# Optimization experiments

Measured on AMD Instinct MI355X. Metric: run time of the kernel, lower is better.

Reference implementation:

```python
import math
import jax, jax.numpy as jnp
import numpy as np

B, T, C, H = 2, 1024, 1024, 16
D = C // H
NEG = -jnp.inf


def setup_inputs() -> dict:
    key = jax.random.key(0)
    ks = jax.random.split(key, 4)
    x_star = jax.random.normal(ks[0], (B, T, C), jnp.float32)
    x_hat = jax.random.normal(ks[1], (B, T, C), jnp.float32)
    # attn_masks semantics: True = keep. star-keys: causal; hat-keys: diagonal only.
    keep_star = jnp.broadcast_to(jnp.tril(jnp.ones((T, T), bool)), (B, T, T))
    keep_hat = jnp.broadcast_to(jnp.eye(T, dtype=bool), (B, T, T))
    W_attn = jax.random.normal(ks[2], (C, 3 * C), jnp.float32) * (1.0 / math.sqrt(C))
    b_attn = jnp.zeros((3 * C,), jnp.float32)
    W_proj = jax.random.normal(ks[3], (C, C), jnp.float32) * (1.0 / math.sqrt(C))
    b_proj = jnp.zeros((C,), jnp.float32)
    return dict(x_star=x_star, x_hat=x_hat, keep_star=keep_star, keep_hat=keep_hat,
                W_attn=W_attn, b_attn=b_attn, W_proj=W_proj, b_proj=b_proj)


def _interleave(x_star, x_hat, keep_star, keep_hat, W_attn, b_attn, W_proj, b_proj):
    def qkv(x):
        q, k, v = jnp.split(x @ W_attn + b_attn, 3, axis=-1)
        r = lambda t: t.reshape(B, T, H, D).transpose(0, 2, 1, 3)  # (B,H,T,D)
        return r(q), r(k), r(v)

    q_s, k_s, v_s = qkv(x_star)
    q_h, k_h, v_h = qkv(x_hat)

    scale = 1.0 / math.sqrt(D)
    attend = lambda q, k: jnp.einsum('bhqd,bhkd->bhqk', q, k) * scale

    # blocking masks (True = block), broadcast over heads
    mask_star = ~keep_star[:, None, :, :]
    mask_hat = ~keep_hat[:, None, :, :]
    mask_causal = ~jnp.tril(jnp.ones((T, T), bool))[None, None]

    def mlp(y):  # (B,H,T,D) -> (B,T,C)
        y = y.transpose(0, 2, 1, 3).reshape(B, T, C)
        return y @ W_proj + b_proj  # resid_dropout is identity in eval

    # star stream: plain causal self-attention
    att_star = jnp.where(mask_causal, NEG, attend(q_s, k_s))
    y_star = mlp(jax.nn.softmax(att_star, axis=-1) @ v_s)

    # hat stream: merge two score streams (hat queries vs star keys / hat keys)
    att_hs = jnp.where(mask_star, NEG, attend(q_h, k_s))
    att_hh = jnp.where(mask_hat, NEG, attend(q_h, k_h))
    merged = jnp.where(jnp.isinf(att_hh), att_hs, att_hh)
    p = jax.nn.softmax(merged, axis=-1)
    y_hat = (jnp.where(mask_star, 0.0, p) @ v_s
             + jnp.where(mask_hat, 0.0, p) @ v_h)
    y_hat = mlp(y_hat)
    return y_star, y_hat


def reference(x_star, x_hat, keep_star, keep_hat, W_attn, b_attn, W_proj, b_proj):
    return _interleave(x_star, x_hat, keep_star, keep_hat, W_attn, b_attn, W_proj, b_proj)
```

## Files before the change

kernel.cpp:

```cpp
#include <hip/hip_runtime.h>
#include <math.h>

#define T_ 1024
#define C_ 1024
#define H_ 16
#define D_ 64
#define B_ 2
#define M2 (B_*T_*C_)
#define QSC 0.18033688f

typedef __attribute__((ext_vector_type(8))) short bf16x8;
typedef __attribute__((ext_vector_type(8))) unsigned short ushort8;
typedef __attribute__((ext_vector_type(4))) float f32x4;

__device__ inline float fast_exp2(float x) {
  return __builtin_amdgcn_exp2f(x);
}

__device__ inline unsigned short f2bf(float f) {
  unsigned int u = __float_as_uint(f);
  u += 0x7fff + ((u >> 16) & 1);
  return (unsigned short)(u >> 16);
}
__device__ inline float bf2f(unsigned short u) {
  return __uint_as_float(((unsigned int)u) << 16);
}
__device__ inline unsigned int pack2bf(float lo, float hi) {
  unsigned int ul = __float_as_uint(lo);
  unsigned int uh = __float_as_uint(hi);
  ul += 0x7fff + ((ul >> 16) & 1);
  uh += 0x7fff + ((uh >> 16) & 1);
  return (ul >> 16) | (uh & 0xffff0000u);
}

__device__ inline void load16(unsigned short* lds, const unsigned short* g) {
  __builtin_amdgcn_global_load_lds(
      (const __attribute__((address_space(1))) unsigned int*)g,
      (__attribute__((address_space(3))) unsigned int*)lds, 16, 0, 0);
}

__device__ void transpose_tile(const float* __restrict__ Win,
                               unsigned short* __restrict__ Wout, int N,
                               int n0, int k0, float (*Ts)[65], int tid)
{
#pragma unroll
  for (int p = 0; p < 4; ++p) {
    int chunk = tid + p * 256;
    int r = chunk >> 4, c4 = chunk & 15;
    float4 v = *(const float4*)(Win + (size_t)(k0 + r) * N + n0 + c4 * 4);
    Ts[r][c4*4+0] = v.x; Ts[r][c4*4+1] = v.y;
    Ts[r][c4*4+2] = v.z; Ts[r][c4*4+3] = v.w;
  }
  __syncthreads();
#pragma unroll
  for (int p = 0; p < 2; ++p) {
    int chunk = tid + p * 256;
    int n = chunk >> 3, kq = chunk & 7;
    ushort8 o;
#pragma unroll
    for (int j = 0; j < 8; ++j) o[j] = f2bf(Ts[kq * 8 + j][n]);
    *(ushort8*)(Wout + (size_t)(n0 + n) * 1024 + k0 + kq * 8) = o;
  }
}

__global__ __launch_bounds__(256) void prepass(
    const float* __restrict__ xs, const float* __restrict__ xh,
    const float* __restrict__ Wa, const float* __restrict__ Wp,
    unsigned short* __restrict__ Xbf, unsigned short* __restrict__ WaT,
    unsigned short* __restrict__ WpT)
{
  __shared__ float Ts[64][65];
  const int bid = blockIdx.x;
  const int tid = threadIdx.x;
  if (bid < 4096) {
    size_t c = (size_t)bid * 256 + tid;
    size_t e = c * 4;
    const float* src = (e < (size_t)2048 * 1024) ? (xs + e)
                                                 : (xh + e - (size_t)2048 * 1024);
    float4 v = *(const float4*)src;
    ushort4 o;
    o.x = f2bf(v.x); o.y = f2bf(v.y); o.z = f2bf(v.z); o.w = f2bf(v.w);
    *(ushort4*)(Xbf + e) = o;
  } else if (bid < 4864) {
    int t = bid - 4096;
    transpose_tile(Wa, WaT, 3072, (t % 48) * 64, (t / 48) * 64, Ts, tid);
  } else {
    int t = bid - 4864;
    transpose_tile(Wp, WpT, 1024, (t % 16) * 64, (t / 16) * 64, Ts, tid);
  }
}

__global__ __launch_bounds__(512) void qkv_mfma(
    const unsigned short* __restrict__ A,
    const unsigned short* __restrict__ Bt,
    const float* __restrict__ bias,
    unsigned short* __restrict__ qkv)
{
  __shared__ __align__(16) unsigned short As[128 * 64];
  __shared__ __align__(16) unsigned short Bs[128 * 64];
  const int tid = threadIdx.x;
  const int col0 = blockIdx.x * 128;
  const int row0 = blockIdx.y * 128;
  const int w = tid >> 6, lane = tid & 63;
  const int lane16 = lane & 15, quad = lane >> 4;
  const int wm = w >> 2, wn = w & 3;
  f32x4 acc[4][2];
#pragma unroll
  for (int mt = 0; mt < 4; ++mt)
#pragma unroll
    for (int nt = 0; nt < 2; ++nt) acc[mt][nt] = (f32x4){0.f, 0.f, 0.f, 0.f};

  for (int k0 = 0; k0 < 1024; k0 += 64) {
    __syncthreads();
#pragma unroll
    for (int it = 0; it < 2; ++it) {
      int chunk = tid + it * 512;
      int row = chunk >> 3, cq = chunk & 7, gq = cq ^ (row & 7);
      load16(As + chunk * 8, A  + (size_t)(row0 + row) * 1024 + k0 + gq * 8);
      load16(Bs + chunk * 8, Bt + (size_t)(col0 + row) * 1024 + k0 + gq * 8);
    }
    __syncthreads();
#pragma unroll
    for (int kb = 0; kb < 2; ++kb) {
      bf16x8 af[4], bfr[2];
      int q = kb * 4 + quad;
#pragma unroll
      for (int mt = 0; mt < 4; ++mt) {
        int m = wm * 64 + mt * 16 + lane16;
        af[mt] = *(const bf16x8*)&As[m * 64 + (q ^ (m & 7)) * 8];
      }
#pragma unroll
      for (int nt = 0; nt < 2; ++nt) {
        int n = wn * 32 + nt * 16 + lane16;
        bfr[nt] = *(const bf16x8*)&Bs[n * 64 + (q ^ (n & 7)) * 8];
      }
#pragma unroll
      for (int mt = 0; mt < 4; ++mt)
#pragma unroll
        for (int nt = 0; nt < 2; ++nt)
          acc[mt][nt] = __builtin_amdgcn_mfma_f32_16x16x32_bf16(
              af[mt], bfr[nt], acc[mt][nt], 0, 0, 0);
    }
  }

#pragma unroll
  for (int mt = 0; mt < 4; ++mt) {
#pragma unroll
    for (int nt = 0; nt < 2; ++nt) {
      int gn = col0 + wn * 32 + nt * 16 + lane16;
      int which = gn >> 10, c = gn & 1023;
      int h = c >> 6, d = c & 63;
      float bv = bias[gn];
#pragma unroll
      for (int r = 0; r < 4; ++r) {
        int gm = row0 + wm * 64 + mt * 16 + quad * 4 + r;
        int s = gm >> 11, b = (gm >> 10) & 1, t = gm & 1023;
        float val = acc[mt][nt][r] + bv;
        if (which == 0) val *= QSC;
        size_t idx;
        if (which == 2 && s == 0)
          idx = (size_t)2 * M2 + ((size_t)(b * 16 + h) * 64 + d) * 1024 + t;
        else
          idx = (size_t)(s * 3 + which) * M2 +
                ((size_t)(b * 16 + h) * 1024 + t) * 64 + d;
        qkv[idx] = f2bf(val);
      }
    }
  }
}

__global__ __launch_bounds__(256) void proj_mfma(
    const unsigned short* __restrict__ A,
    const unsigned short* __restrict__ Bt,
    const float* __restrict__ bias,
    float* __restrict__ out)
{
  __shared__ __align__(16) unsigned short As[128 * 64];
  __shared__ __align__(16) unsigned short Bs[64 * 64];
  const int tid = threadIdx.x;
  const int col0 = blockIdx.x * 64;
  const int row0 = blockIdx.y * 128;
  const int w = tid >> 6, lane = tid & 63;
  const int lane16 = lane & 15, quad = lane >> 4;
  const int wm = w >> 1, wn = w & 1;
  f32x4 acc[4][2];
#pragma unroll
  for (int mt = 0; mt < 4; ++mt)
#pragma unroll
    for (int nt = 0; nt < 2; ++nt) acc[mt][nt] = (f32x4){0.f, 0.f, 0.f, 0.f};

  for (int k0 = 0; k0 < 1024; k0 += 64) {
    __syncthreads();
#pragma unroll
    for (int it = 0; it < 4; ++it) {
      int chunk = tid + it * 256;
      int row = chunk >> 3, cq = chunk & 7, gq = cq ^ (row & 7);
      load16(As + chunk * 8, A + (size_t)(row0 + row) * 1024 + k0 + gq * 8);
    }
#pragma unroll
    for (int it = 0; it < 2; ++it) {
      int chunk = tid + it * 256;
      int row = chunk >> 3, cq = chunk & 7, gq = cq ^ (row & 7);
      load16(Bs + chunk * 8, Bt + (size_t)(col0 + row) * 1024 + k0 + gq * 8);
    }
    __syncthreads();
#pragma unroll
    for (int kb = 0; kb < 2; ++kb) {
      bf16x8 af[4], bfr[2];
      int q = kb * 4 + quad;
#pragma unroll
      for (int mt = 0; mt < 4; ++mt) {
        int m = wm * 64 + mt * 16 + lane16;
        af[mt] = *(const bf16x8*)&As[m * 64 + (q ^ (m & 7)) * 8];
      }
#pragma unroll
      for (int nt = 0; nt < 2; ++nt) {
        int n = wn * 32 + nt * 16 + lane16;
        bfr[nt] = *(const bf16x8*)&Bs[n * 64 + (q ^ (n & 7)) * 8];
      }
#pragma unroll
      for (int mt = 0; mt < 4; ++mt)
#pragma unroll
        for (int nt = 0; nt < 2; ++nt)
          acc[mt][nt] = __builtin_amdgcn_mfma_f32_16x16x32_bf16(
              af[mt], bfr[nt], acc[mt][nt], 0, 0, 0);
    }
  }

#pragma unroll
  for (int mt = 0; mt < 4; ++mt) {
#pragma unroll
    for (int nt = 0; nt < 2; ++nt) {
      int gn = col0 + wn * 32 + nt * 16 + lane16;
      float bv = bias[gn];
#pragma unroll
      for (int r = 0; r < 4; ++r) {
        int gm = row0 + wm * 64 + mt * 16 + quad * 4 + r;
        out[(size_t)gm * 1024 + gn] = acc[mt][nt][r] + bv;
      }
    }
  }
}

__global__ __launch_bounds__(256) void attn_kernel(
    const unsigned short* __restrict__ ws, unsigned short* __restrict__ Y)
{
  __shared__ __align__(16) unsigned short Qs[64 * 64];
  __shared__ __align__(16) unsigned short Ks[2][64 * 64];
  __shared__ __align__(16) unsigned short Vts[2][64 * 64];
  __shared__ __align__(16) unsigned short Ps[4][16][72];
  __shared__ float diag[64];

  const int tid = threadIdx.x;
  const int bx  = blockIdx.x;
  const int inner = bx & 63;
  const int h = inner & 15;
  const int b = (inner >> 4) & 1;
  const int s = (inner >> 5) & 1;
  const int qt = 15 - (bx >> 6);
  const int i0 = qt * 64;
  const size_t hb = (size_t)(b * H_ + h) * T_ * D_;

  const unsigned short* Qg  = ws + (size_t)(s ? 3 : 0) * M2 + hb;
  const unsigned short* Kg  = ws + (size_t)1 * M2 + hb;
  const unsigned short* VTg = ws + (size_t)2 * M2 + hb;
  const unsigned short* Khg = ws + (size_t)4 * M2 + hb;
  const unsigned short* Vhg = ws + (size_t)5 * M2 + hb;

  const int lane = tid & 63;
  const int w = tid >> 6;
  const int lane16 = lane & 15, quad = lane >> 4;
  const int wq0 = w * 16;

#pragma unroll
  for (int it = 0; it < 2; ++it) {
    int ch = tid + it * 256;
    int row = ch >> 3, cq = ch & 7, gq = cq ^ (row & 7);
    load16(Qs + ch * 8, Qg + (size_t)(i0 + row) * 64 + gq * 8);
    load16(&Ks[0][ch * 8], Kg + (size_t)(0 * 64 + row) * 64 + gq * 8);
    load16(&Vts[0][ch * 8], VTg + (size_t)row * 1024 + 0 * 64 + gq * 8);
  }
  __syncthreads();

  bf16x8 qf[2];
  {
    int m = wq0 + lane16;
    qf[0] = *(const bf16x8*)&Qs[m * 64 + ((quad) ^ (m & 7)) * 8];
    qf[1] = *(const bf16x8*)&Qs[m * 64 + ((4 + quad) ^ (m & 7)) * 8];
  }
  if (s == 1) {
    if (tid < 64) {
      const unsigned short* kh = Khg + (size_t)(i0 + tid) * 64;
      float sum = 0.f;
#pragma unroll
      for (int c = 0; c < 8; ++c) {
        bf16x8 qv = *(const bf16x8*)&Qs[tid * 64 + (c ^ (tid & 7)) * 8];
        ushort8 kv = *(const ushort8*)(kh + c * 8);
#pragma unroll
        for (int j = 0; j < 8; ++j)
          sum += bf2f((unsigned short)qv[j]) * bf2f(kv[j]);
      }
      diag[tid] = sum;
    }
    __syncthreads();
  }

  float mrun = -INFINITY, lrun = 0.f;
  f32x4 O[4];
#pragma unroll
  for (int nt = 0; nt < 4; ++nt) O[nt] = (f32x4){0.f, 0.f, 0.f, 0.f};

  for (int kt = 0; kt <= qt; ++kt) {
    const int cur = kt & 1;
    if (kt < qt) {
      const int nxt = 1 - cur;
#pragma unroll
      for (int it = 0; it < 2; ++it) {
        int ch = tid + it * 256;
        int row = ch >> 3, cq = ch & 7, gq = cq ^ (row & 7);
        load16(&Ks[nxt][ch * 8], Kg + (size_t)((kt + 1) * 64 + row) * 64 + gq * 8);
        load16(&Vts[nxt][ch * 8], VTg + (size_t)row * 1024 + (kt + 1) * 64 + gq * 8);
      }
    }

    f32x4 St[4];
#pragma unroll
    for (int mt = 0; mt < 4; ++mt) St[mt] = (f32x4){0.f, 0.f, 0.f, 0.f};
#pragma unroll
    for (int kb = 0; kb < 2; ++kb) {
#pragma unroll
      for (int mt = 0; mt < 4; ++mt) {
        int m = mt * 16 + lane16;
        bf16x8 kf = *(const bf16x8*)&Ks[cur][m * 64 + ((kb * 4 + quad) ^ (m & 7)) * 8];
        St[mt] = __builtin_amdgcn_mfma_f32_16x16x32_bf16(kf, qf[kb], St[mt], 0, 0, 0);
      }
    }

    if (kt == qt) {
      const int kstar = wq0 + lane16;
      const float dv = (s == 1) ? diag[kstar] : 0.f;
#pragma unroll
      for (int mt = 0; mt < 4; ++mt)
#pragma unroll
        for (int r = 0; r < 4; ++r) {
          int key = mt * 16 + quad * 4 + r;
          float v = St[mt][r];
          if (s == 1 && key == kstar) v = dv;
          if (key > kstar) v = -INFINITY;
          St[mt][r] = v;
        }
    }

    float mt_ = -INFINITY;
#pragma unroll
    for (int mt = 0; mt < 4; ++mt)
#pragma unroll
      for (int r = 0; r < 4; ++r) mt_ = fmaxf(mt_, St[mt][r]);
    mt_ = fmaxf(mt_, __shfl_xor(mt_, 16, 64));
    mt_ = fmaxf(mt_, __shfl_xor(mt_, 32, 64));
    float mnew = fmaxf(mrun, mt_);
    float alpha = fast_exp2(mrun - mnew);
    mrun = mnew;
    float rsum = 0.f;
#pragma unroll
    for (int mt = 0; mt < 4; ++mt)
#pragma unroll
      for (int r = 0; r < 4; ++r) {
        float p = fast_exp2(St[mt][r] - mnew);
        St[mt][r] = p;
        rsum += p;
      }
    rsum += __shfl_xor(rsum, 16, 64);
    rsum += __shfl_xor(rsum, 32, 64);
    lrun = lrun * alpha + rsum;

#pragma unroll
    for (int mt = 0; mt < 4; ++mt) {
      *(unsigned int*)&Ps[w][lane16][mt * 16 + quad * 4] =
          pack2bf(St[mt][0], St[mt][1]);
      *(unsigned int*)&Ps[w][lane16][mt * 16 + quad * 4 + 2] =
          pack2bf(St[mt][2], St[mt][3]);
    }

    float a4[4];
#pragma unroll
    for (int r = 0; r < 4; ++r) a4[r] = __shfl(alpha, quad * 4 + r, 16);
#pragma unroll
    for (int nt = 0; nt < 4; ++nt)
#pragma unroll
      for (int r = 0; r < 4; ++r) O[nt][r] *= a4[r];

#pragma unroll
    for (int kb = 0; kb < 2; ++kb) {
      bf16x8 pa = *(const bf16x8*)&Ps[w][lane16][kb * 32 + quad * 8];
#pragma unroll
      for (int nt = 0; nt < 4; ++nt) {
        int n = nt * 16 + lane16;
        bf16x8 vb = *(const bf16x8*)&Vts[cur][n * 64 + ((kb * 4 + quad) ^ (n & 7)) * 8];
        O[nt] = __builtin_amdgcn_mfma_f32_16x16x32_bf16(pa, vb, O[nt], 0, 0, 0);
      }
    }

    if (s == 1 && kt == qt) {
      float pd = fast_exp2(diag[wq0 + lane16] - mrun);
      float p4[4];
#pragma unroll
      for (int r = 0; r < 4; ++r) p4[r] = __shfl(pd, quad * 4 + r, 16);
#pragma unroll
      for (int r = 0; r < 4; ++r) {
        const unsigned short* vh = Vhg + (size_t)(i0 + wq0 + quad * 4 + r) * 64;
#pragma unroll
        for (int nt = 0; nt < 4; ++nt)
          O[nt][r] += p4[r] * bf2f(vh[nt * 16 + lane16]);
      }
    }
    __syncthreads();
  }

  float l4[4];
#pragma unroll
  for (int r = 0; r < 4; ++r) l4[r] = __shfl(lrun, quad * 4 + r, 16);
#pragma unroll
  for (int r = 0; r < 4; ++r) {
    int gi = i0 + wq0 + quad * 4 + r;
    float inv = 1.f / l4[r];
    unsigned short* yo = Y + ((size_t)(s * 2048 + b * 1024 + gi)) * 1024 + h * 64;
#pragma unroll
    for (int nt = 0; nt < 4; ++nt)
      yo[nt * 16 + lane16] = f2bf(O[nt][r] * inv);
  }
}

extern "C" void kernel_launch(void* const* d_in, const int* in_sizes, int n_in,
                              void* d_out, int out_size, void* d_ws, size_t ws_size,
                              hipStream_t stream) {
  (void)in_sizes; (void)n_in; (void)out_size; (void)ws_size;
  const float* xs = (const float*)d_in[0];
  const float* xh = (const float*)d_in[1];
  const float* Wa = (const float*)d_in[4];
  const float* ba = (const float*)d_in[5];
  const float* Wp = (const float*)d_in[6];
  const float* bp = (const float*)d_in[7];

  unsigned short* qkv = (unsigned short*)d_ws;
  unsigned short* Ybf = qkv + (size_t)6 * M2;
  unsigned short* Xbf = Ybf + (size_t)4 * 1024 * 1024;
  unsigned short* WaT = Xbf + (size_t)4 * 1024 * 1024;
  unsigned short* WpT = WaT + (size_t)3 * 1024 * 1024;
  float* out = (float*)d_out;

  prepass    <<<5120, 256, 0, stream>>>(xs, xh, Wa, Wp, Xbf, WaT, WpT);
  qkv_mfma   <<<dim3(24, 32), 512, 0, stream>>>(Xbf, WaT, ba, qkv);
  attn_kernel<<<dim3(1024), 256, 0, stream>>>(qkv, Ybf);
  proj_mfma  <<<dim3(16, 32), 256, 0, stream>>>(Ybf, WpT, bp, out);
}
```

Measured before the change: 181.4 us.

## Fuse star and hat attention streams into one block sharing K/V tiles

The attention kernel now runs the star and hat query streams for the same (batch, head, query tile) inside one block. Each K and V^T tile is loaded into shared memory and fragments once, then used by both streams, which halves the block count and the K/V global traffic. The cost is about twice the registers per thread (two output accumulators, preloaded K/V fragments) and half as many blocks, so occupancy and load balance across the causal triangle may suffer.

```diff
diff --git a/kernel.cpp b/kernel.cpp
--- a/kernel.cpp
+++ b/kernel.cpp
@@ -242,10 +242,11 @@
   }
 }
 
-__global__ __launch_bounds__(256) void attn_kernel(
+__global__ __launch_bounds__(256) void attn_fused(
     const unsigned short* __restrict__ ws, unsigned short* __restrict__ Y)
 {
-  __shared__ __align__(16) unsigned short Qs[64 * 64];
+  __shared__ __align__(16) unsigned short Qss[64 * 64];
+  __shared__ __align__(16) unsigned short Qsh[64 * 64];
   __shared__ __align__(16) unsigned short Ks[2][64 * 64];
   __shared__ __align__(16) unsigned short Vts[2][64 * 64];
   __shared__ __align__(16) unsigned short Ps[4][16][72];
@@ -253,17 +254,17 @@
 
   const int tid = threadIdx.x;
   const int bx  = blockIdx.x;
-  const int inner = bx & 63;
+  const int inner = bx & 31;
   const int h = inner & 15;
   const int b = (inner >> 4) & 1;
-  const int s = (inner >> 5) & 1;
-  const int qt = 15 - (bx >> 6);
+  const int qt = 15 - (bx >> 5);
   const int i0 = qt * 64;
   const size_t hb = (size_t)(b * H_ + h) * T_ * D_;
 
-  const unsigned short* Qg  = ws + (size_t)(s ? 3 : 0) * M2 + hb;
+  const unsigned short* Qsg = ws + (size_t)0 * M2 + hb;
   const unsigned short* Kg  = ws + (size_t)1 * M2 + hb;
   const unsigned short* VTg = ws + (size_t)2 * M2 + hb;
+  const unsigned short* Qhg = ws + (size_t)3 * M2 + hb;
   const unsigned short* Khg = ws + (size_t)4 * M2 + hb;
   const unsigned short* Vhg = ws + (size_t)5 * M2 + hb;
 
@@ -276,39 +277,45 @@
   for (int it = 0; it < 2; ++it) {
     int ch = tid + it * 256;
     int row = ch >> 3, cq = ch & 7, gq = cq ^ (row & 7);
-    load16(Qs + ch * 8, Qg + (size_t)(i0 + row) * 64 + gq * 8);
-    load16(&Ks[0][ch * 8], Kg + (size_t)(0 * 64 + row) * 64 + gq * 8);
-    load16(&Vts[0][ch * 8], VTg + (size_t)row * 1024 + 0 * 64 + gq * 8);
+    load16(Qss + ch * 8, Qsg + (size_t)(i0 + row) * 64 + gq * 8);
+    load16(Qsh + ch * 8, Qhg + (size_t)(i0 + row) * 64 + gq * 8);
+    load16(&Ks[0][ch * 8], Kg + (size_t)row * 64 + gq * 8);
+    load16(&Vts[0][ch * 8], VTg + (size_t)row * 1024 + gq * 8);
   }
   __syncthreads();
 
-  bf16x8 qf[2];
+  bf16x8 qfs[2], qfh[2];
   {
     int m = wq0 + lane16;
-    qf[0] = *(const bf16x8*)&Qs[m * 64 + ((quad) ^ (m & 7)) * 8];
-    qf[1] = *(const bf16x8*)&Qs[m * 64 + ((4 + quad) ^ (m & 7)) * 8];
-  }
-  if (s == 1) {
-    if (tid < 64) {
-      const unsigned short* kh = Khg + (size_t)(i0 + tid) * 64;
-      float sum = 0.f;
-#pragma unroll
-      for (int c = 0; c < 8; ++c) {
-        bf16x8 qv = *(const bf16x8*)&Qs[tid * 64 + (c ^ (tid & 7)) * 8];
-        ushort8 kv = *(const ushort8*)(kh + c * 8);
-#pragma unroll
-        for (int j = 0; j < 8; ++j)
-          sum += bf2f((unsigned short)qv[j]) * bf2f(kv[j]);
-      }
-      diag[tid] = sum;
-    }
-    __syncthreads();
-  }
-
-  float mrun = -INFINITY, lrun = 0.f;
-  f32x4 O[4];
-#pragma unroll
-  for (int nt = 0; nt < 4; ++nt) O[nt] = (f32x4){0.f, 0.f, 0.f, 0.f};
+    qfs[0] = *(const bf16x8*)&Qss[m * 64 + ((quad) ^ (m & 7)) * 8];
+    qfs[1] = *(const bf16x8*)&Qss[m * 64 + ((4 + quad) ^ (m & 7)) * 8];
+    qfh[0] = *(const bf16x8*)&Qsh[m * 64 + ((quad) ^ (m & 7)) * 8];
+    qfh[1] = *(const bf16x8*)&Qsh[m * 64 + ((4 + quad) ^ (m & 7)) * 8];
+  }
+  if (tid < 64) {
+    const unsigned short* kh = Khg + (size_t)(i0 + tid) * 64;
+    float sum = 0.f;
+#pragma unroll
+    for (int c = 0; c < 8; ++c) {
+      bf16x8 qv = *(const bf16x8*)&Qsh[tid * 64 + (c ^ (tid & 7)) * 8];
+      ushort8 kv = *(const ushort8*)(kh + c * 8);
+#pragma unroll
+      for (int j = 0; j < 8; ++j)
+        sum += bf2f((unsigned short)qv[j]) * bf2f(kv[j]);
+    }
+    diag[tid] = sum;
+  }
+  __syncthreads();
+
+  float mrun_s = -INFINITY, lrun_s = 0.f;
+  float mrun_h = -INFINITY, lrun_h = 0.f;
+  f32x4 Os[4], Oh[4];
+#pragma unroll
+  for (int nt = 0; nt < 4; ++nt) {
+    Os[nt] = (f32x4){0.f, 0.f, 0.f, 0.f};
+    Oh[nt] = (f32x4){0.f, 0.f, 0.f, 0.f};
+  }
+  const int kstar = wq0 + lane16;
 
   for (int kt = 0; kt <= qt; ++kt) {
     const int cur = kt & 1;
@@ -323,111 +330,190 @@
       }
     }
 
-    f32x4 St[4];
-#pragma unroll
-    for (int mt = 0; mt < 4; ++mt) St[mt] = (f32x4){0.f, 0.f, 0.f, 0.f};
+    bf16x8 kf[2][4], vf[2][4];
 #pragma unroll
     for (int kb = 0; kb < 2; ++kb) {
+      int q = kb * 4 + quad;
 #pragma unroll
       for (int mt = 0; mt < 4; ++mt) {
         int m = mt * 16 + lane16;
-        bf16x8 kf = *(const bf16x8*)&Ks[cur][m * 64 + ((kb * 4 + quad) ^ (m & 7)) * 8];
-        St[mt] = __builtin_amdgcn_mfma_f32_16x16x32_bf16(kf, qf[kb], St[mt], 0, 0, 0);
-      }
-    }
-
-    if (kt == qt) {
-      const int kstar = wq0 + lane16;
-      const float dv = (s == 1) ? diag[kstar] : 0.f;
+        kf[kb][mt] = *(const bf16x8*)&Ks[cur][m * 64 + (q ^ (m & 7)) * 8];
+        vf[kb][mt] = *(const bf16x8*)&Vts[cur][m * 64 + (q ^ (m & 7)) * 8];
+      }
+    }
+
+    {
+      f32x4 St[4];
+#pragma unroll
+      for (int mt = 0; mt < 4; ++mt) St[mt] = (f32x4){0.f, 0.f, 0.f, 0.f};
+#pragma unroll
+      for (int kb = 0; kb < 2; ++kb)
+#pragma unroll
+        for (int mt = 0; mt < 4; ++mt)
+          St[mt] = __builtin_amdgcn_mfma_f32_16x16x32_bf16(
+              kf[kb][mt], qfs[kb], St[mt], 0, 0, 0);
+
+      if (kt == qt) {
+#pragma unroll
+        for (int mt = 0; mt < 4; ++mt)
+#pragma unroll
+          for (int r = 0; r < 4; ++r)
+            if (mt * 16 + quad * 4 + r > kstar) St[mt][r] = -INFINITY;
+      }
+
+      float mt_ = -INFINITY;
 #pragma unroll
       for (int mt = 0; mt < 4; ++mt)
 #pragma unroll
+        for (int r = 0; r < 4; ++r) mt_ = fmaxf(mt_, St[mt][r]);
+      mt_ = fmaxf(mt_, __shfl_xor(mt_, 16, 64));
+      mt_ = fmaxf(mt_, __shfl_xor(mt_, 32, 64));
+      float mnew = fmaxf(mrun_s, mt_);
+      float alpha = fast_exp2(mrun_s - mnew);
+      mrun_s = mnew;
+      float rsum = 0.f;
+#pragma unroll
+      for (int mt = 0; mt < 4; ++mt)
+#pragma unroll
         for (int r = 0; r < 4; ++r) {
-          int key = mt * 16 + quad * 4 + r;
-          float v = St[mt][r];
-          if (s == 1 && key == kstar) v = dv;
-          if (key > kstar) v = -INFINITY;
-          St[mt][r] = v;
+          float p = fast_exp2(St[mt][r] - mnew);
+          St[mt][r] = p;
+          rsum += p;
         }
-    }
-
-    float mt_ = -INFINITY;
-#pragma unroll
-    for (int mt = 0; mt < 4; ++mt)
-#pragma unroll
-      for (int r = 0; r < 4; ++r) mt_ = fmaxf(mt_, St[mt][r]);
-    mt_ = fmaxf(mt_, __shfl_xor(mt_, 16, 64));
-    mt_ = fmaxf(mt_, __shfl_xor(mt_, 32, 64));
-    float mnew = fmaxf(mrun, mt_);
-    float alpha = fast_exp2(mrun - mnew);
-    mrun = mnew;
-    float rsum = 0.f;
-#pragma unroll
-    for (int mt = 0; mt < 4; ++mt)
-#pragma unroll
-      for (int r = 0; r < 4; ++r) {
-        float p = fast_exp2(St[mt][r] - mnew);
-        St[mt][r] = p;
-        rsum += p;
-      }
-    rsum += __shfl_xor(rsum, 16, 64);
-    rsum += __shfl_xor(rsum, 32, 64);
-    lrun = lrun * alpha + rsum;
-
-#pragma unroll
-    for (int mt = 0; mt < 4; ++mt) {
-      *(unsigned int*)&Ps[w][lane16][mt * 16 + quad * 4] =
-          pack2bf(St[mt][0], St[mt][1]);
-      *(unsigned int*)&Ps[w][lane16][mt * 16 + quad * 4 + 2] =
-          pack2bf(St[mt][2], St[mt][3]);
-    }
-
-    float a4[4];
-#pragma unroll
-    for (int r = 0; r < 4; ++r) a4[r] = __shfl(alpha, quad * 4 + r, 16);
-#pragma unroll
-    for (int nt = 0; nt < 4; ++nt)
-#pragma unroll
-      for (int r = 0; r < 4; ++r) O[nt][r] *= a4[r];
-
-#pragma unroll
-    for (int kb = 0; kb < 2; ++kb) {
-      bf16x8 pa = *(const bf16x8*)&Ps[w][lane16][kb * 32 + quad * 8];
-#pragma unroll
-      for (int nt = 0; nt < 4; ++nt) {
-        int n = nt * 16 + lane16;
-        bf16x8 vb = *(const bf16x8*)&Vts[cur][n * 64 + ((kb * 4 + quad) ^ (n & 7)) * 8];
-        O[nt] = __builtin_amdgcn_mfma_f32_16x16x32_bf16(pa, vb, O[nt], 0, 0, 0);
-      }
-    }
-
-    if (s == 1 && kt == qt) {
-      float pd = fast_exp2(diag[wq0 + lane16] - mrun);
-      float p4[4];
-#pragma unroll
-      for (int r = 0; r < 4; ++r) p4[r] = __shfl(pd, quad * 4 + r, 16);
-#pragma unroll
-      for (int r = 0; r < 4; ++r) {
-        const unsigned short* vh = Vhg + (size_t)(i0 + wq0 + quad * 4 + r) * 64;
+      rsum += __shfl_xor(rsum, 16, 64);
+      rsum += __shfl_xor(rsum, 32, 64);
+      lrun_s = lrun_s * alpha + rsum;
+
+#pragma unroll
+      for (int mt = 0; mt < 4; ++mt) {
+        *(unsigned int*)&Ps[w][lane16][mt * 16 + quad * 4] =
+            pack2bf(St[mt][0], St[mt][1]);
+        *(unsigned int*)&Ps[w][lane16][mt * 16 + quad * 4 + 2] =
+            pack2bf(St[mt][2], St[mt][3]);
+      }
+      float a4[4];
+#pragma unroll
+      for (int r = 0; r < 4; ++r) a4[r] = __shfl(alpha, quad * 4 + r, 16);
+#pragma unroll
+      for (int nt = 0; nt < 4; ++nt)
+#pragma unroll
+        for (int r = 0; r < 4; ++r) Os[nt][r] *= a4[r];
+#pragma unroll
+      for (int kb = 0; kb < 2; ++kb) {
+        bf16x8 pa = *(const bf16x8*)&Ps[w][lane16][kb * 32 + quad * 8];
 #pragma unroll
         for (int nt = 0; nt < 4; ++nt)
-          O[nt][r] += p4[r] * bf2f(vh[nt * 16 + lane16]);
+          Os[nt] = __builtin_amdgcn_mfma_f32_16x16x32_bf16(
+              pa, vf[kb][nt], Os[nt], 0, 0, 0);
+      }
+    }
+
+    {
+      f32x4 St[4];
+#pragma unroll
+      for (int mt = 0; mt < 4; ++mt) St[mt] = (f32x4){0.f, 0.f, 0.f, 0.f};
+#pragma unroll
+      for (int kb = 0; kb < 2; ++kb)
+#pragma unroll
+        for (int mt = 0; mt < 4; ++mt)
+          St[mt] = __builtin_amdgcn_mfma_f32_16x16x32_bf16(
+              kf[kb][mt], qfh[kb], St[mt], 0, 0, 0);
+
+      if (kt == qt) {
+        const float dv = diag[kstar];
+#pragma unroll
+        for (int mt = 0; mt < 4; ++mt)
+#pragma unroll
+          for (int r = 0; r < 4; ++r) {
+            int key = mt * 16 + quad * 4 + r;
+            float v = St[mt][r];
+            if (key == kstar) v = dv;
+            if (key > kstar) v = -INFINITY;
+            St[mt][r] = v;
+          }
+      }
+
+      float mt_ = -INFINITY;
+#pragma unroll
+      for (int mt = 0; mt < 4; ++mt)
+#pragma unroll
+        for (int r = 0; r < 4; ++r) mt_ = fmaxf(mt_, St[mt][r]);
+      mt_ = fmaxf(mt_, __shfl_xor(mt_, 16, 64));
+      mt_ = fmaxf(mt_, __shfl_xor(mt_, 32, 64));
+      float mnew = fmaxf(mrun_h, mt_);
+      float alpha = fast_exp2(mrun_h - mnew);
+      mrun_h = mnew;
+      float rsum = 0.f;
+#pragma unroll
+      for (int mt = 0; mt < 4; ++mt)
+#pragma unroll
+        for (int r = 0; r < 4; ++r) {
+          float p = fast_exp2(St[mt][r] - mnew);
+          St[mt][r] = p;
+          rsum += p;
+        }
+      rsum += __shfl_xor(rsum, 16, 64);
+      rsum += __shfl_xor(rsum, 32, 64);
+      lrun_h = lrun_h * alpha + rsum;
+
+#pragma unroll
+      for (int mt = 0; mt < 4; ++mt) {
+        *(unsigned int*)&Ps[w][lane16][mt * 16 + quad * 4] =
+            pack2bf(St[mt][0], St[mt][1]);
+        *(unsigned int*)&Ps[w][lane16][mt * 16 + quad * 4 + 2] =
+            pack2bf(St[mt][2], St[mt][3]);
+      }
+      float a4[4];
+#pragma unroll
+      for (int r = 0; r < 4; ++r) a4[r] = __shfl(alpha, quad * 4 + r, 16);
+#pragma unroll
+      for (int nt = 0; nt < 4; ++nt)
+#pragma unroll
+        for (int r = 0; r < 4; ++r) Oh[nt][r] *= a4[r];
+#pragma unroll
+      for (int kb = 0; kb < 2; ++kb) {
+        bf16x8 pa = *(const bf16x8*)&Ps[w][lane16][kb * 32 + quad * 8];
+#pragma unroll
+        for (int nt = 0; nt < 4; ++nt)
+          Oh[nt] = __builtin_amdgcn_mfma_f32_16x16x32_bf16(
+              pa, vf[kb][nt], Oh[nt], 0, 0, 0);
+      }
+
+      if (kt == qt) {
+        float pd = fast_exp2(diag[kstar] - mrun_h);
+        float p4[4];
+#pragma unroll
+        for (int r = 0; r < 4; ++r) p4[r] = __shfl(pd, quad * 4 + r, 16);
+#pragma unroll
+        for (int r = 0; r < 4; ++r) {
+          const unsigned short* vh = Vhg + (size_t)(i0 + wq0 + quad * 4 + r) * 64;
+#pragma unroll
+          for (int nt = 0; nt < 4; ++nt)
+            Oh[nt][r] += p4[r] * bf2f(vh[nt * 16 + lane16]);
+        }
       }
     }
     __syncthreads();
   }
 
-  float l4[4];
-#pragma unroll
-  for (int r = 0; r < 4; ++r) l4[r] = __shfl(lrun, quad * 4 + r, 16);
+  float ls4[4], lh4[4];
+#pragma unroll
+  for (int r = 0; r < 4; ++r) {
+    ls4[r] = __shfl(lrun_s, quad * 4 + r, 16);
+    lh4[r] = __shfl(lrun_h, quad * 4 + r, 16);
+  }
 #pragma unroll
   for (int r = 0; r < 4; ++r) {
     int gi = i0 + wq0 + quad * 4 + r;
-    float inv = 1.f / l4[r];
-    unsigned short* yo = Y + ((size_t)(s * 2048 + b * 1024 + gi)) * 1024 + h * 64;
-#pragma unroll
-    for (int nt = 0; nt < 4; ++nt)
-      yo[nt * 16 + lane16] = f2bf(O[nt][r] * inv);
+    float invs = 1.f / ls4[r];
+    float invh = 1.f / lh4[r];
+    unsigned short* ys = Y + ((size_t)(b * 1024 + gi)) * 1024 + h * 64;
+    unsigned short* yh = Y + ((size_t)(2048 + b * 1024 + gi)) * 1024 + h * 64;
+#pragma unroll
+    for (int nt = 0; nt < 4; ++nt) {
+      ys[nt * 16 + lane16] = f2bf(Os[nt][r] * invs);
+      yh[nt * 16 + lane16] = f2bf(Oh[nt][r] * invh);
+    }
   }
 }
 
@@ -449,8 +535,8 @@
   unsigned short* WpT = WaT + (size_t)3 * 1024 * 1024;
   float* out = (float*)d_out;
 
-  prepass    <<<5120, 256, 0, stream>>>(xs, xh, Wa, Wp, Xbf, WaT, WpT);
-  qkv_mfma   <<<dim3(24, 32), 512, 0, stream>>>(Xbf, WaT, ba, qkv);
-  attn_kernel<<<dim3(1024), 256, 0, stream>>>(qkv, Ybf);
-  proj_mfma  <<<dim3(16, 32), 256, 0, stream>>>(Ybf, WpT, bp, out);
-}
+  prepass   <<<5120, 256, 0, stream>>>(xs, xh, Wa, Wp, Xbf, WaT, WpT);
+  qkv_mfma  <<<dim3(24, 32), 512, 0, stream>>>(Xbf, WaT, ba, qkv);
+  attn_fused<<<dim3(512), 256, 0, stream>>>(qkv, Ybf);
+  proj_mfma <<<dim3(16, 32), 256, 0, stream>>>(Ybf, WpT, bp, out);
+}
```

Measured after the change: 182.0 us. Within noise of the previous version (+0.3%).

## Fuse star and hat attention streams into one block sharing K/V tiles

Applied to the files above, without the earlier changes.

The attention kernel now handles the star and hat query streams for the same (batch, head, query tile) in a single block. It loads each star K/V tile once and uses it for both streams, keeping two sets of softmax state and accumulators. This halves the grid and removes the duplicated K/V global loads and LDS staging that separate blocks needed. In exchange, register and LDS use per block rise, occupancy may drop, and with only 512 blocks under a causal imbalance, load balance across CUs may suffer.

```diff
diff --git a/kernel.cpp b/kernel.cpp
--- a/kernel.cpp
+++ b/kernel.cpp
@@ -242,28 +242,29 @@
   }
 }
 
-__global__ __launch_bounds__(256) void attn_kernel(
+__global__ __launch_bounds__(256) void attn_fused(
     const unsigned short* __restrict__ ws, unsigned short* __restrict__ Y)
 {
-  __shared__ __align__(16) unsigned short Qs[64 * 64];
+  __shared__ __align__(16) unsigned short Qss[64 * 64];
+  __shared__ __align__(16) unsigned short Qsh[64 * 64];
   __shared__ __align__(16) unsigned short Ks[2][64 * 64];
   __shared__ __align__(16) unsigned short Vts[2][64 * 64];
-  __shared__ __align__(16) unsigned short Ps[4][16][72];
+  __shared__ __align__(16) unsigned short Ps[4][2][16][72];
   __shared__ float diag[64];
 
   const int tid = threadIdx.x;
   const int bx  = blockIdx.x;
-  const int inner = bx & 63;
+  const int inner = bx & 31;
   const int h = inner & 15;
   const int b = (inner >> 4) & 1;
-  const int s = (inner >> 5) & 1;
-  const int qt = 15 - (bx >> 6);
+  const int qt = 15 - (bx >> 5);
   const int i0 = qt * 64;
   const size_t hb = (size_t)(b * H_ + h) * T_ * D_;
 
-  const unsigned short* Qg  = ws + (size_t)(s ? 3 : 0) * M2 + hb;
+  const unsigned short* Qsg = ws + (size_t)0 * M2 + hb;
   const unsigned short* Kg  = ws + (size_t)1 * M2 + hb;
   const unsigned short* VTg = ws + (size_t)2 * M2 + hb;
+  const unsigned short* Qhg = ws + (size_t)3 * M2 + hb;
   const unsigned short* Khg = ws + (size_t)4 * M2 + hb;
   const unsigned short* Vhg = ws + (size_t)5 * M2 + hb;
 
@@ -276,39 +277,44 @@
   for (int it = 0; it < 2; ++it) {
     int ch = tid + it * 256;
     int row = ch >> 3, cq = ch & 7, gq = cq ^ (row & 7);
-    load16(Qs + ch * 8, Qg + (size_t)(i0 + row) * 64 + gq * 8);
-    load16(&Ks[0][ch * 8], Kg + (size_t)(0 * 64 + row) * 64 + gq * 8);
-    load16(&Vts[0][ch * 8], VTg + (size_t)row * 1024 + 0 * 64 + gq * 8);
+    load16(Qss + ch * 8, Qsg + (size_t)(i0 + row) * 64 + gq * 8);
+    load16(Qsh + ch * 8, Qhg + (size_t)(i0 + row) * 64 + gq * 8);
+    load16(&Ks[0][ch * 8], Kg + (size_t)row * 64 + gq * 8);
+    load16(&Vts[0][ch * 8], VTg + (size_t)row * 1024 + gq * 8);
   }
   __syncthreads();
 
-  bf16x8 qf[2];
+  bf16x8 qf[2][2];
   {
     int m = wq0 + lane16;
-    qf[0] = *(const bf16x8*)&Qs[m * 64 + ((quad) ^ (m & 7)) * 8];
-    qf[1] = *(const bf16x8*)&Qs[m * 64 + ((4 + quad) ^ (m & 7)) * 8];
-  }
-  if (s == 1) {
-    if (tid < 64) {
-      const unsigned short* kh = Khg + (size_t)(i0 + tid) * 64;
-      float sum = 0.f;
-#pragma unroll
-      for (int c = 0; c < 8; ++c) {
-        bf16x8 qv = *(const bf16x8*)&Qs[tid * 64 + (c ^ (tid & 7)) * 8];
-        ushort8 kv = *(const ushort8*)(kh + c * 8);
-#pragma unroll
-        for (int j = 0; j < 8; ++j)
-          sum += bf2f((unsigned short)qv[j]) * bf2f(kv[j]);
-      }
-      diag[tid] = sum;
-    }
-    __syncthreads();
-  }
-
-  float mrun = -INFINITY, lrun = 0.f;
-  f32x4 O[4];
-#pragma unroll
-  for (int nt = 0; nt < 4; ++nt) O[nt] = (f32x4){0.f, 0.f, 0.f, 0.f};
+    qf[0][0] = *(const bf16x8*)&Qss[m * 64 + ((quad) ^ (m & 7)) * 8];
+    qf[0][1] = *(const bf16x8*)&Qss[m * 64 + ((4 + quad) ^ (m & 7)) * 8];
+    qf[1][0] = *(const bf16x8*)&Qsh[m * 64 + ((quad) ^ (m & 7)) * 8];
+    qf[1][1] = *(const bf16x8*)&Qsh[m * 64 + ((4 + quad) ^ (m & 7)) * 8];
+  }
+  if (tid < 64) {
+    const unsigned short* kh = Khg + (size_t)(i0 + tid) * 64;
+    float sum = 0.f;
+#pragma unroll
+    for (int c = 0; c < 8; ++c) {
+      bf16x8 qv = *(const bf16x8*)&Qsh[tid * 64 + (c ^ (tid & 7)) * 8];
+      ushort8 kv = *(const ushort8*)(kh + c * 8);
+#pragma unroll
+      for (int j = 0; j < 8; ++j)
+        sum += bf2f((unsigned short)qv[j]) * bf2f(kv[j]);
+    }
+    diag[tid] = sum;
+  }
+  __syncthreads();
+
+  float mrun[2] = {-INFINITY, -INFINITY};
+  float lrun[2] = {0.f, 0.f};
+  f32x4 O[2][4];
+#pragma unroll
+  for (int st = 0; st < 2; ++st)
+#pragma unroll
+    for (int nt = 0; nt < 4; ++nt) O[st][nt] = (f32x4){0.f, 0.f, 0.f, 0.f};
+  const int kstar = wq0 + lane16;
 
   for (int kt = 0; kt <= qt; ++kt) {
     const int cur = kt & 1;
@@ -323,86 +329,108 @@
       }
     }
 
-    f32x4 St[4];
-#pragma unroll
-    for (int mt = 0; mt < 4; ++mt) St[mt] = (f32x4){0.f, 0.f, 0.f, 0.f};
+    bf16x8 kf[2][4], vf[2][4];
 #pragma unroll
     for (int kb = 0; kb < 2; ++kb) {
+      int q = kb * 4 + quad;
 #pragma unroll
       for (int mt = 0; mt < 4; ++mt) {
         int m = mt * 16 + lane16;
-        bf16x8 kf = *(const bf16x8*)&Ks[cur][m * 64 + ((kb * 4 + quad) ^ (m & 7)) * 8];
-        St[mt] = __builtin_amdgcn_mfma_f32_16x16x32_bf16(kf, qf[kb], St[mt], 0, 0, 0);
-      }
-    }
+        kf[kb][mt] = *(const bf16x8*)&Ks[cur][m * 64 + (q ^ (m & 7)) * 8];
+        vf[kb][mt] = *(const bf16x8*)&Vts[cur][m * 64 + (q ^ (m & 7)) * 8];
+      }
+    }
+
+    f32x4 St[2][4];
+#pragma unroll
+    for (int st = 0; st < 2; ++st)
+#pragma unroll
+      for (int mt = 0; mt < 4; ++mt) St[st][mt] = (f32x4){0.f, 0.f, 0.f, 0.f};
+#pragma unroll
+    for (int kb = 0; kb < 2; ++kb)
+#pragma unroll
+      for (int st = 0; st < 2; ++st)
+#pragma unroll
+        for (int mt = 0; mt < 4; ++mt)
+          St[st][mt] = __builtin_amdgcn_mfma_f32_16x16x32_bf16(
+              kf[kb][mt], qf[st][kb], St[st][mt], 0, 0, 0);
 
     if (kt == qt) {
-      const int kstar = wq0 + lane16;
-      const float dv = (s == 1) ? diag[kstar] : 0.f;
+      const float dv = diag[kstar];
 #pragma unroll
       for (int mt = 0; mt < 4; ++mt)
 #pragma unroll
         for (int r = 0; r < 4; ++r) {
           int key = mt * 16 + quad * 4 + r;
-          float v = St[mt][r];
-          if (s == 1 && key == kstar) v = dv;
-          if (key > kstar) v = -INFINITY;
-          St[mt][r] = v;
+          if (key > kstar) { St[0][mt][r] = -INFINITY; St[1][mt][r] = -INFINITY; }
+          if (key == kstar) St[1][mt][r] = dv;
         }
     }
 
-    float mt_ = -INFINITY;
-#pragma unroll
-    for (int mt = 0; mt < 4; ++mt)
-#pragma unroll
-      for (int r = 0; r < 4; ++r) mt_ = fmaxf(mt_, St[mt][r]);
-    mt_ = fmaxf(mt_, __shfl_xor(mt_, 16, 64));
-    mt_ = fmaxf(mt_, __shfl_xor(mt_, 32, 64));
-    float mnew = fmaxf(mrun, mt_);
-    float alpha = fast_exp2(mrun - mnew);
-    mrun = mnew;
-    float rsum = 0.f;
-#pragma unroll
-    for (int mt = 0; mt < 4; ++mt)
-#pragma unroll
-      for (int r = 0; r < 4; ++r) {
-        float p = fast_exp2(St[mt][r] - mnew);
-        St[mt][r] = p;
-        rsum += p;
-      }
-    rsum += __shfl_xor(rsum, 16, 64);
-    rsum += __shfl_xor(rsum, 32, 64);
-    lrun = lrun * alpha + rsum;
-
-#pragma unroll
-    for (int mt = 0; mt < 4; ++mt) {
-      *(unsigned int*)&Ps[w][lane16][mt * 16 + quad * 4] =
-          pack2bf(St[mt][0], St[mt][1]);
-      *(unsigned int*)&Ps[w][lane16][mt * 16 + quad * 4 + 2] =
-          pack2bf(St[mt][2], St[mt][3]);
-    }
-
-    float a4[4];
-#pragma unroll
-    for (int r = 0; r < 4; ++r) a4[r] = __shfl(alpha, quad * 4 + r, 16);
-#pragma unroll
-    for (int nt = 0; nt < 4; ++nt)
-#pragma unroll
-      for (int r = 0; r < 4; ++r) O[nt][r] *= a4[r];
+    float alpha[2];
+#pragma unroll
+    for (int st = 0; st < 2; ++st) {
+      float mt_ = -INFINITY;
+#pragma unroll
+      for (int mt = 0; mt < 4; ++mt)
+#pragma unroll
+        for (int r = 0; r < 4; ++r) mt_ = fmaxf(mt_, St[st][mt][r]);
+      mt_ = fmaxf(mt_, __shfl_xor(mt_, 16, 64));
+      mt_ = fmaxf(mt_, __shfl_xor(mt_, 32, 64));
+      float mnew = fmaxf(mrun[st], mt_);
+      alpha[st] = fast_exp2(mrun[st] - mnew);
+      mrun[st] = mnew;
+      float rsum = 0.f;
+#pragma unroll
+      for (int mt = 0; mt < 4; ++mt)
+#pragma unroll
+        for (int r = 0; r < 4; ++r) {
+          float p = fast_exp2(St[st][mt][r] - mnew);
+          St[st][mt][r] = p;
+          rsum += p;
+        }
+      rsum += __shfl_xor(rsum, 16, 64);
+      rsum += __shfl_xor(rsum, 32, 64);
+      lrun[st] = lrun[st] * alpha[st] + rsum;
+    }
+
+#pragma unroll
+    for (int st = 0; st < 2; ++st)
+#pragma unroll
+      for (int mt = 0; mt < 4; ++mt) {
+        *(unsigned int*)&Ps[w][st][lane16][mt * 16 + quad * 4] =
+            pack2bf(St[st][mt][0], St[st][mt][1]);
+        *(unsigned int*)&Ps[w][st][lane16][mt * 16 + quad * 4 + 2] =
+            pack2bf(St[st][mt][2], St[st][mt][3]);
+      }
+
+#pragma unroll
+    for (int st = 0; st < 2; ++st) {
+      float a4[4];
+#pragma unroll
+      for (int r = 0; r < 4; ++r) a4[r] = __shfl(alpha[st], quad * 4 + r, 16);
+#pragma unroll
+      for (int nt = 0; nt < 4; ++nt)
+#pragma unroll
+        for (int r = 0; r < 4; ++r) O[st][nt][r] *= a4[r];
+    }
 
 #pragma unroll
     for (int kb = 0; kb < 2; ++kb) {
-      bf16x8 pa = *(const bf16x8*)&Ps[w][lane16][kb * 32 + quad * 8];
-#pragma unroll
-      for (int nt = 0; nt < 4; ++nt) {
-        int n = nt * 16 + lane16;
-        bf16x8 vb = *(const bf16x8*)&Vts[cur][n * 64 + ((kb * 4 + quad) ^ (n & 7)) * 8];
-        O[nt] = __builtin_amdgcn_mfma_f32_16x16x32_bf16(pa, vb, O[nt], 0, 0, 0);
-      }
-    }
-
-    if (s == 1 && kt == qt) {
-      float pd = fast_exp2(diag[wq0 + lane16] - mrun);
+      bf16x8 pa[2];
+#pragma unroll
+      for (int st = 0; st < 2; ++st)
+        pa[st] = *(const bf16x8*)&Ps[w][st][lane16][kb * 32 + quad * 8];
+#pragma unroll
+      for (int st = 0; st < 2; ++st)
+#pragma unroll
+        for (int nt = 0; nt < 4; ++nt)
+          O[st][nt] = __builtin_amdgcn_mfma_f32_16x16x32_bf16(
+              pa[st], vf[kb][nt], O[st][nt], 0, 0, 0);
+    }
+
+    if (kt == qt) {
+      float pd = fast_exp2(diag[kstar] - mrun[1]);
       float p4[4];
 #pragma unroll
       for (int r = 0; r < 4; ++r) p4[r] = __shfl(pd, quad * 4 + r, 16);
@@ -411,23 +439,30 @@
         const unsigned short* vh = Vhg + (size_t)(i0 + wq0 + quad * 4 + r) * 64;
 #pragma unroll
         for (int nt = 0; nt < 4; ++nt)
-          O[nt][r] += p4[r] * bf2f(vh[nt * 16 + lane16]);
+          O[1][nt][r] += p4[r] * bf2f(vh[nt * 16 + lane16]);
       }
     }
     __syncthreads();
   }
 
-  float l4[4];
-#pragma unroll
-  for (int r = 0; r < 4; ++r) l4[r] = __shfl(lrun, quad * 4 + r, 16);
+  float l4[2][4];
+#pragma unroll
+  for (int st = 0; st < 2; ++st)
+#pragma unroll
+    for (int r = 0; r < 4; ++r)
+      l4[st][r] = __shfl(lrun[st], quad * 4 + r, 16);
 #pragma unroll
   for (int r = 0; r < 4; ++r) {
     int gi = i0 + wq0 + quad * 4 + r;
-    float inv = 1.f / l4[r];
-    unsigned short* yo = Y + ((size_t)(s * 2048 + b * 1024 + gi)) * 1024 + h * 64;
-#pragma unroll
-    for (int nt = 0; nt < 4; ++nt)
-      yo[nt * 16 + lane16] = f2bf(O[nt][r] * inv);
+    float invs = 1.f / l4[0][r];
+    float invh = 1.f / l4[1][r];
+    unsigned short* ys = Y + ((size_t)(b * 1024 + gi)) * 1024 + h * 64;
+    unsigned short* yh = Y + ((size_t)(2048 + b * 1024 + gi)) * 1024 + h * 64;
+#pragma unroll
+    for (int nt = 0; nt < 4; ++nt) {
+      ys[nt * 16 + lane16] = f2bf(O[0][nt][r] * invs);
+      yh[nt * 16 + lane16] = f2bf(O[1][nt][r] * invh);
+    }
   }
 }
 
@@ -449,8 +484,8 @@
   unsigned short* WpT = WaT + (size_t)3 * 1024 * 1024;
   float* out = (float*)d_out;
 
-  prepass    <<<5120, 256, 0, stream>>>(xs, xh, Wa, Wp, Xbf, WaT, WpT);
-  qkv_mfma   <<<dim3(24, 32), 512, 0, stream>>>(Xbf, WaT, ba, qkv);
-  attn_kernel<<<dim3(1024), 256, 0, stream>>>(qkv, Ybf);
-  proj_mfma  <<<dim3(16, 32), 256, 0, stream>>>(Ybf, WpT, bp, out);
-}
+  prepass   <<<5120, 256, 0, stream>>>(xs, xh, Wa, Wp, Xbf, WaT, WpT);
+  qkv_mfma  <<<dim3(24, 32), 512, 0, stream>>>(Xbf, WaT, ba, qkv);
+  attn_fused<<<dim3(512), 256, 0, stream>>>(qkv, Ybf);
+  proj_mfma <<<dim3(16, 32), 256, 0, stream>>>(Ybf, WpT, bp, out);
+}
```

New measurement: 184.4 us. Within noise of the previous version (+1.6%).
